# Kernel optimization log

Measured on AMD Instinct MI355X. Metric: run time of the kernel, lower is better.

Reference implementation:

```python
import jax, jax.numpy as jnp
import numpy as np

HEAD_SIZE = 1024
NUM_HEADS = 8
D_K = HEAD_SIZE // NUM_HEADS  # only used as the softmax scale; no head split in this module
B, S = 8, 2048


def setup_inputs() -> dict:
    key = jax.random.key(0)
    ks = jax.random.split(key, 11)
    d = HEAD_SIZE
    scale = 1.0 / np.sqrt(d)
    inp = {
        'query': jax.random.normal(ks[0], (B, S, d), dtype=jnp.float32),
        'key': jax.random.normal(ks[1], (B, S, d), dtype=jnp.float32),
        'value': jax.random.normal(ks[2], (B, S, d), dtype=jnp.float32),
        'Wq': jax.random.normal(ks[3], (d, d), dtype=jnp.float32) * scale,
        'bq': jnp.zeros((d,), dtype=jnp.float32),
        'Wk': jax.random.normal(ks[4], (d, d), dtype=jnp.float32) * scale,
        'bk': jnp.zeros((d,), dtype=jnp.float32),
        'Wv': jax.random.normal(ks[5], (d, d), dtype=jnp.float32) * scale,
        'bv': jnp.zeros((d,), dtype=jnp.float32),
        'Wo': jax.random.normal(ks[6], (d, d), dtype=jnp.float32) * scale,
        'bo': jnp.zeros((d,), dtype=jnp.float32),
    }
    return inp


def reference(query, key, value, Wq, bq, Wk, bk, Wv, bv, Wo, bo):
    # per-input linear projections (torch Linear: x @ W.T + b)
    q = jnp.einsum('bsd,ed->bse', query, Wq) + bq
    k = jnp.einsum('bsd,ed->bse', key, Wk) + bk
    v = jnp.einsum('bsd,ed->bse', value, Wv) + bv
    # NOTE: no head split in the original module; scale uses d_k = head_size/num_heads
    scores = jnp.einsum('bqd,bkd->bqk', q, k) / jnp.sqrt(jnp.float32(D_K))
    p_attn = jax.nn.softmax(scores, axis=-1)  # [B, S, S]
    x = jnp.einsum('bqk,bkd->bqd', p_attn, v)
    out = jnp.einsum('bsd,ed->bse', x, Wo) + bo
    return out
```

## Files before the change

### kernel.cpp

```cpp
#include <hip/hip_runtime.h>
#include <hip/hip_bf16.h>
#include <math.h>

typedef __bf16 bf16_t;
typedef _Float16 f16_t;
typedef bf16_t bf16x8 __attribute__((ext_vector_type(8)));
typedef bf16_t bf16x4 __attribute__((ext_vector_type(4)));
typedef f16_t  f16x8  __attribute__((ext_vector_type(8)));
typedef f16_t  f16x4  __attribute__((ext_vector_type(4)));
typedef float  f32x4  __attribute__((ext_vector_type(4)));

__global__ __launch_bounds__(256) void cvt_f32_bf16(
    const float* __restrict__ in, bf16_t* __restrict__ out, int n4) {
  int i = blockIdx.x * 256 + threadIdx.x;
  if (i >= n4) return;
  float4 v = ((const float4*)in)[i];
  bf16x4 o;
  o[0] = (bf16_t)v.x; o[1] = (bf16_t)v.y; o[2] = (bf16_t)v.z; o[3] = (bf16_t)v.w;
  ((bf16x4*)out)[i] = o;
}

__global__ __launch_bounds__(256) void transpose_bf16(
    const bf16_t* __restrict__ in, bf16_t* __restrict__ out, int R, int C) {
  __shared__ bf16_t t[64][65];
  size_t boff = (size_t)blockIdx.z * R * C;
  in += boff; out += boff;
  int r0 = blockIdx.y * 64, c0 = blockIdx.x * 64;
  int x = threadIdx.x & 63, y4 = threadIdx.x >> 6;
  #pragma unroll
  for (int yy = y4; yy < 64; yy += 4)
    t[yy][x] = in[(size_t)(r0 + yy) * C + c0 + x];
  __syncthreads();
  #pragma unroll
  for (int yy = y4; yy < 64; yy += 4)
    out[(size_t)(c0 + yy) * R + r0 + x] = t[x][yy];
}

__global__ __launch_bounds__(256) void softmax_rows_f16(f16_t* __restrict__ sc) {
  f16_t* rp = sc + (size_t)blockIdx.x * 2048;
  int tid = threadIdx.x;
  f16x8 v = ((const f16x8*)rp)[tid];
  float f[8];
  #pragma unroll
  for (int t = 0; t < 8; t++) f[t] = (float)v[t];

  float m = f[0];
  #pragma unroll
  for (int t = 1; t < 8; t++) m = fmaxf(m, f[t]);
  #pragma unroll
  for (int o = 32; o; o >>= 1) m = fmaxf(m, __shfl_xor(m, o));
  __shared__ float redm[4];
  if ((tid & 63) == 0) redm[tid >> 6] = m;
  __syncthreads();
  m = fmaxf(fmaxf(redm[0], redm[1]), fmaxf(redm[2], redm[3]));

  float s = 0.f;
  #pragma unroll
  for (int t = 0; t < 8; t++) { f[t] = __expf(f[t] - m); s += f[t]; }
  #pragma unroll
  for (int o = 32; o; o >>= 1) s += __shfl_xor(s, o);
  __shared__ float reds[4];
  if ((tid & 63) == 0) reds[tid >> 6] = s;
  __syncthreads();
  s = reds[0] + reds[1] + reds[2] + reds[3];
  float inv = 1.0f / s;

  bf16x8 o8;
  #pragma unroll
  for (int t = 0; t < 8; t++) o8[t] = (bf16_t)(f[t] * inv);
  ((bf16x8*)rp)[tid] = o8;
}

__device__ __forceinline__ void store4(float* p, float4 v) { *(float4*)p = v; }
__device__ __forceinline__ void store4(bf16_t* p, float4 v) {
  bf16x4 o; o[0] = (bf16_t)v.x; o[1] = (bf16_t)v.y;
  o[2] = (bf16_t)v.z; o[3] = (bf16_t)v.w; *(bf16x4*)p = o;
}
__device__ __forceinline__ void store4(f16_t* p, float4 v) {
  f16x4 o; o[0] = (f16_t)v.x; o[1] = (f16_t)v.y;
  o[2] = (f16_t)v.z; o[3] = (f16_t)v.w; *(f16x4*)p = o;
}

#define TM 128
#define TN 128
#define TK 64

__device__ __forceinline__ void load16_lds(const bf16_t* g, bf16_t* l) {
  __builtin_amdgcn_global_load_lds(
      (__attribute__((address_space(1))) void*)const_cast<bf16_t*>(g),
      (__attribute__((address_space(3))) void*)l, 16, 0, 0);
}

template <typename CT>
__global__ __launch_bounds__(256, 2) void gemm_bt(
    const bf16_t* __restrict__ A, int lda, size_t strA,
    const bf16_t* __restrict__ B, int ldb, size_t strB,
    CT* __restrict__ C, int ldc, size_t strC,
    const float* __restrict__ bias, float scale,
    int M, int N, int K) {
  __shared__ __align__(16) char smem[2][(TM * TK + TN * TK) * 2];

  A += (size_t)blockIdx.z * strA;
  B += (size_t)blockIdx.z * strB;
  C += (size_t)blockIdx.z * strC;
  int m0 = blockIdx.x * TM;
  int n0 = blockIdx.y * TN;
  int tid  = threadIdx.x;
  int lane = tid & 63;
  int wv   = tid >> 6;
  int wrow = wv >> 1;
  int wcol = wv & 1;

  f32x4 acc[4][4];
  #pragma unroll
  for (int i = 0; i < 4; i++)
    #pragma unroll
    for (int j = 0; j < 4; j++) acc[i][j] = (f32x4)0.f;

  int lrow = lane & 15;
  int lk   = (lane >> 4) * 8;

  auto stage = [&](int k0, int buf) {
    bf16_t* As = (bf16_t*)smem[buf];
    bf16_t* Bs = As + TM * TK;
    #pragma unroll
    for (int i = 0; i < 4; i++) {
      int chunk  = i * 4096 + wv * 1024;
      int lchunk = chunk + lane * 16;
      int row = lchunk >> 7;
      int kb  = (lchunk & 127) >> 1;
      load16_lds(A + (size_t)(m0 + row) * lda + k0 + kb, As + (chunk >> 1));
      load16_lds(B + (size_t)(n0 + row) * ldb + k0 + kb, Bs + (chunk >> 1));
    }
  };

  int nk = K / TK;
  stage(0, 0);
  __syncthreads();

  for (int kk = 0; kk < nk; kk++) {
    if (kk + 1 < nk) stage((kk + 1) * TK, (kk + 1) & 1);

    const bf16_t* As = (const bf16_t*)smem[kk & 1];
    const bf16_t* Bs = As + TM * TK;
    #pragma unroll
    for (int ks = 0; ks < TK; ks += 32) {
      bf16x8 af[4], bfr[4];
      #pragma unroll
      for (int i = 0; i < 4; i++)
        af[i] = *(const bf16x8*)&As[(wrow * 64 + i * 16 + lrow) * TK + ks + lk];
      #pragma unroll
      for (int j = 0; j < 4; j++)
        bfr[j] = *(const bf16x8*)&Bs[(wcol * 64 + j * 16 + lrow) * TK + ks + lk];
      #pragma unroll
      for (int i = 0; i < 4; i++)
        #pragma unroll
        for (int j = 0; j < 4; j++)
          acc[i][j] = __builtin_amdgcn_mfma_f32_16x16x32_bf16(af[i], bfr[j],
                                                              acc[i][j], 0, 0, 0);
    }
    __syncthreads();
  }

  float* Cs = (float*)smem[0];
  #pragma unroll
  for (int h = 0; h < 2; h++) {
    __syncthreads();
    if (wrow == h) {
      #pragma unroll
      for (int i = 0; i < 4; i++) {
        int lr = i * 16 + (lane >> 4) * 4;
        #pragma unroll
        for (int j = 0; j < 4; j++) {
          int lc = wcol * 64 + j * 16 + (lane & 15);
          #pragma unroll
          for (int r = 0; r < 4; r++)
            Cs[(lr + r) * 128 + lc] = acc[i][j][r];
        }
      }
    }
    __syncthreads();
    #pragma unroll
    for (int io = 0; io < 8; io++) {
      int idx = io * 256 + tid;
      int r   = idx >> 5;
      int c4  = (idx & 31) * 4;
      float4 v = *(const float4*)&Cs[r * 128 + c4];
      int grow = m0 + h * 64 + r;
      int gcol = n0 + c4;
      float4 bv = bias ? *(const float4*)&bias[gcol] : make_float4(0, 0, 0, 0);
      v.x = v.x * scale + bv.x; v.y = v.y * scale + bv.y;
      v.z = v.z * scale + bv.z; v.w = v.w * scale + bv.w;
      store4(C + (size_t)grow * ldc + gcol, v);
    }
  }
}

extern "C" void kernel_launch(void* const* d_in, const int* in_sizes, int n_in,
                              void* d_out, int out_size, void* d_ws, size_t ws_size,
                              hipStream_t stream) {
  const float* query = (const float*)d_in[0];
  const float* key_  = (const float*)d_in[1];
  const float* value = (const float*)d_in[2];
  const float* Wq = (const float*)d_in[3];
  const float* bq = (const float*)d_in[4];
  const float* Wk = (const float*)d_in[5];
  const float* bk = (const float*)d_in[6];
  const float* Wv = (const float*)d_in[7];
  const float* bv = (const float*)d_in[8];
  const float* Wo = (const float*)d_in[9];
  const float* bo = (const float*)d_in[10];
  float* out = (float*)d_out;

  const int Bb = 8, S = 2048, D = 1024;
  const int MS = Bb * S;
  const size_t ND = (size_t)MS * D;
  const size_t WD = (size_t)D * D;

  char* ws = (char*)d_ws;
  bf16_t* Wqb = (bf16_t*)ws;
  bf16_t* Wkb = Wqb + WD;
  bf16_t* Wvb = Wkb + WD;
  bf16_t* Wob = Wvb + WD;
  f16_t*  SC  = (f16_t*)(Wob + WD);
  bf16_t* IN  = (bf16_t*)SC;
  bf16_t* Qb  = (bf16_t*)((char*)SC + (size_t)Bb * S * S * 2);
  bf16_t* Kb  = Qb + ND;
  bf16_t* VT  = Kb;
  bf16_t* Xb  = Kb + ND;

  const int n4i = (int)(ND / 4), n4w = (int)(WD / 4);

  cvt_f32_bf16<<<dim3(n4w / 256), 256, 0, stream>>>(Wq, Wqb, n4w);
  cvt_f32_bf16<<<dim3(n4w / 256), 256, 0, stream>>>(Wk, Wkb, n4w);
  cvt_f32_bf16<<<dim3(n4w / 256), 256, 0, stream>>>(Wv, Wvb, n4w);
  cvt_f32_bf16<<<dim3(n4w / 256), 256, 0, stream>>>(Wo, Wob, n4w);

  dim3 pgrid(MS / TM, D / TN, 1);
  cvt_f32_bf16<<<dim3(n4i / 256), 256, 0, stream>>>(query, IN, n4i);
  gemm_bt<bf16_t><<<pgrid, 256, 0, stream>>>(
      IN, D, 0, Wqb, D, 0, Qb, D, 0, bq, 1.f, MS, D, D);
  cvt_f32_bf16<<<dim3(n4i / 256), 256, 0, stream>>>(key_, IN, n4i);
  gemm_bt<bf16_t><<<pgrid, 256, 0, stream>>>(
      IN, D, 0, Wkb, D, 0, Kb, D, 0, bk, 1.f, MS, D, D);
  cvt_f32_bf16<<<dim3(n4i / 256), 256, 0, stream>>>(value, IN, n4i);
  gemm_bt<bf16_t><<<pgrid, 256, 0, stream>>>(
      IN, D, 0, Wvb, D, 0, Xb, D, 0, bv, 1.f, MS, D, D);

  gemm_bt<f16_t><<<dim3(S / TM, S / TN, Bb), 256, 0, stream>>>(
      Qb, D, (size_t)S * D, Kb, D, (size_t)S * D, SC, S, (size_t)S * S,
      nullptr, 0.08838834764831845f, S, S, D);

  transpose_bf16<<<dim3(D / 64, S / 64, Bb), 256, 0, stream>>>(Xb, VT, S, D);

  softmax_rows_f16<<<dim3(Bb * S), 256, 0, stream>>>(SC);

  gemm_bt<bf16_t><<<dim3(S / TM, D / TN, Bb), 256, 0, stream>>>(
      (const bf16_t*)SC, S, (size_t)S * S, VT, S, (size_t)D * S,
      Xb, D, (size_t)S * D, nullptr, 1.f, S, D, S);

  gemm_bt<float><<<pgrid, 256, 0, stream>>>(
      Xb, D, 0, Wob, D, 0, out, D, 0, bo, 1.f, MS, D, D);
}
```

Before: 674.4 us.

## Replace 128x128 GEMM with 256x256 tile 8-wave kernel with swizzled LDS pipeline

Replaces the 128x128x64 GEMM with a 256x256x64 tile kernel using 512 threads (8 waves). It also adds an XOR-swizzled LDS layout, staging split into quarter-tile halves interleaved with MFMA phases under s_setprio, and manual waitcnt/barrier scheduling. Batched GEMMs put the batch index on blockIdx.x for better L2 locality. The aim is higher arithmetic intensity and overlap of global loads with MFMA. The cost is 128KB of LDS per block and higher register pressure, which may limit occupancy.

```diff
diff --git a/kernel.cpp b/kernel.cpp
--- a/kernel.cpp
+++ b/kernel.cpp
@@ -81,9 +81,9 @@
   o[2] = (f16_t)v.z; o[3] = (f16_t)v.w; *(f16x4*)p = o;
 }
 
-#define TM 128
-#define TN 128
-#define TK 64
+#define BM 256
+#define BN 256
+#define BK 64
 
 __device__ __forceinline__ void load16_lds(const bf16_t* g, bf16_t* l) {
   __builtin_amdgcn_global_load_lds(
@@ -92,101 +92,183 @@
 }
 
 template <typename CT>
-__global__ __launch_bounds__(256, 2) void gemm_bt(
+__global__ __launch_bounds__(512, 2) void gemm256(
     const bf16_t* __restrict__ A, int lda, size_t strA,
     const bf16_t* __restrict__ B, int ldb, size_t strB,
     CT* __restrict__ C, int ldc, size_t strC,
     const float* __restrict__ bias, float scale,
-    int M, int N, int K) {
-  __shared__ __align__(16) char smem[2][(TM * TK + TN * TK) * 2];
-
-  A += (size_t)blockIdx.z * strA;
-  B += (size_t)blockIdx.z * strB;
-  C += (size_t)blockIdx.z * strC;
-  int m0 = blockIdx.x * TM;
-  int n0 = blockIdx.y * TN;
+    int K, int batch_on_x) {
+  __shared__ __align__(16) char smem[2][65536];
+
+  int bz, mt, nt;
+  if (batch_on_x) { bz = blockIdx.x; nt = blockIdx.y; mt = blockIdx.z; }
+  else            { mt = blockIdx.x; nt = blockIdx.y; bz = blockIdx.z; }
+  A += (size_t)bz * strA;
+  B += (size_t)bz * strB;
+  C += (size_t)bz * strC;
+  int m0 = mt * BM, n0 = nt * BN;
   int tid  = threadIdx.x;
-  int lane = tid & 63;
-  int wv   = tid >> 6;
-  int wrow = wv >> 1;
-  int wcol = wv & 1;
-
-  f32x4 acc[4][4];
-  #pragma unroll
-  for (int i = 0; i < 4; i++)
+  int lane = tid & 63, wv = tid >> 6;
+  int wrow = wv >> 2;
+  int wcol = wv & 3;
+
+  f32x4 acc[8][4];
+  #pragma unroll
+  for (int i = 0; i < 8; i++)
     #pragma unroll
     for (int j = 0; j < 4; j++) acc[i][j] = (f32x4)0.f;
 
   int lrow = lane & 15;
-  int lk   = (lane >> 4) * 8;
-
-  auto stage = [&](int k0, int buf) {
-    bf16_t* As = (bf16_t*)smem[buf];
-    bf16_t* Bs = As + TM * TK;
-    #pragma unroll
-    for (int i = 0; i < 4; i++) {
-      int chunk  = i * 4096 + wv * 1024;
-      int lchunk = chunk + lane * 16;
-      int row = lchunk >> 7;
-      int kb  = (lchunk & 127) >> 1;
-      load16_lds(A + (size_t)(m0 + row) * lda + k0 + kb, As + (chunk >> 1));
-      load16_lds(B + (size_t)(n0 + row) * ldb + k0 + kb, Bs + (chunk >> 1));
+  int lk8  = (lane >> 4) * 8;
+  int xm   = (lrow & 8) << 2;
+
+  auto rd = [&](const char* base, int blk16, int kcol) -> bf16x8 {
+    int byte = (((blk16 << 1) + (kcol >> 5)) << 10)
+             + (lrow << 6) + (((kcol & 31) << 1) ^ xm);
+    return *(const bf16x8*)(base + byte);
+  };
+
+  auto stage_half = [&](int h) {
+    int th = h >> 2, hf = h & 3;
+    char* dstb = smem[th & 1] + hf * 16384;
+    const bf16_t* g; int rb, ld;
+    if (hf < 2) { g = A; rb = m0 + hf * 128;       ld = lda; }
+    else        { g = B; rb = n0 + (hf - 2) * 128; ld = ldb; }
+    int k0 = th * BK;
+    #pragma unroll
+    for (int q = 0; q < 2; q++) {
+      int l = q * 8192 + wv * 1024 + lane * 16;
+      int inner = l & 1023, s = l >> 10;
+      int rl   = ((s >> 1) << 4) | (inner >> 6);
+      int colb = (inner & 63) ^ (((inner >> 9) & 1) << 5);
+      int col  = ((s & 1) << 5) | (colb >> 1);
+      load16_lds(g + (size_t)(rb + rl) * ld + k0 + col,
+                 (bf16_t*)(dstb + q * 8192 + wv * 1024));
     }
   };
 
-  int nk = K / TK;
-  stage(0, 0);
-  __syncthreads();
-
-  for (int kk = 0; kk < nk; kk++) {
-    if (kk + 1 < nk) stage((kk + 1) * TK, (kk + 1) & 1);
-
-    const bf16_t* As = (const bf16_t*)smem[kk & 1];
-    const bf16_t* Bs = As + TM * TK;
-    #pragma unroll
-    for (int ks = 0; ks < TK; ks += 32) {
-      bf16x8 af[4], bfr[4];
-      #pragma unroll
-      for (int i = 0; i < 4; i++)
-        af[i] = *(const bf16x8*)&As[(wrow * 64 + i * 16 + lrow) * TK + ks + lk];
-      #pragma unroll
-      for (int j = 0; j < 4; j++)
-        bfr[j] = *(const bf16x8*)&Bs[(wcol * 64 + j * 16 + lrow) * TK + ks + lk];
-      #pragma unroll
-      for (int i = 0; i < 4; i++)
-        #pragma unroll
-        for (int j = 0; j < 4; j++)
-          acc[i][j] = __builtin_amdgcn_mfma_f32_16x16x32_bf16(af[i], bfr[j],
-                                                              acc[i][j], 0, 0, 0);
-    }
+  int nk = K / BK;
+
+  #pragma unroll
+  for (int h = 0; h < 6; ++h)
+    if (h < 4 * nk) stage_half(h);
+  asm volatile("s_waitcnt vmcnt(4)" ::: "memory");
+  asm volatile("s_barrier" ::: "memory");
+
+  bf16x8 a0[4][2], a1[4][2], bb[2][2];
+
+  for (int t = 0; t < nk; ++t) {
+    const char* Ab = smem[t & 1];
+    const char* Bb = smem[t & 1] + 32768;
+    int hb = 4 * t + 6;
+
+    #pragma unroll
+    for (int i = 0; i < 4; ++i)
+      #pragma unroll
+      for (int s = 0; s < 2; ++s)
+        a0[i][s] = rd(Ab, wrow * 8 + i, s * 32 + lk8);
+    #pragma unroll
+    for (int j = 0; j < 2; ++j)
+      #pragma unroll
+      for (int s = 0; s < 2; ++s)
+        bb[j][s] = rd(Bb, wcol * 4 + j, s * 32 + lk8);
+    if (hb + 0 < 4 * nk) stage_half(hb + 0);
+    asm volatile("s_barrier" ::: "memory");
+    asm volatile("s_waitcnt lgkmcnt(0)");
+    __builtin_amdgcn_s_setprio(1);
+    #pragma unroll
+    for (int i = 0; i < 4; ++i)
+      #pragma unroll
+      for (int j = 0; j < 2; ++j)
+        #pragma unroll
+        for (int s = 0; s < 2; ++s)
+          acc[i][j] = __builtin_amdgcn_mfma_f32_16x16x32_bf16(
+              a0[i][s], bb[j][s], acc[i][j], 0, 0, 0);
+    __builtin_amdgcn_s_setprio(0);
+    asm volatile("s_barrier" ::: "memory");
+
+    #pragma unroll
+    for (int i = 0; i < 4; ++i)
+      #pragma unroll
+      for (int s = 0; s < 2; ++s)
+        a1[i][s] = rd(Ab, wrow * 8 + 4 + i, s * 32 + lk8);
+    if (hb + 1 < 4 * nk) stage_half(hb + 1);
+    asm volatile("s_barrier" ::: "memory");
+    asm volatile("s_waitcnt lgkmcnt(0)");
+    __builtin_amdgcn_s_setprio(1);
+    #pragma unroll
+    for (int i = 0; i < 4; ++i)
+      #pragma unroll
+      for (int j = 0; j < 2; ++j)
+        #pragma unroll
+        for (int s = 0; s < 2; ++s)
+          acc[4 + i][j] = __builtin_amdgcn_mfma_f32_16x16x32_bf16(
+              a1[i][s], bb[j][s], acc[4 + i][j], 0, 0, 0);
+    __builtin_amdgcn_s_setprio(0);
+    asm volatile("s_barrier" ::: "memory");
+
+    #pragma unroll
+    for (int j = 0; j < 2; ++j)
+      #pragma unroll
+      for (int s = 0; s < 2; ++s)
+        bb[j][s] = rd(Bb, wcol * 4 + 2 + j, s * 32 + lk8);
+    if (hb + 2 < 4 * nk) stage_half(hb + 2);
+    asm volatile("s_barrier" ::: "memory");
+    asm volatile("s_waitcnt lgkmcnt(0)");
+    __builtin_amdgcn_s_setprio(1);
+    #pragma unroll
+    for (int i = 0; i < 4; ++i)
+      #pragma unroll
+      for (int j = 0; j < 2; ++j)
+        #pragma unroll
+        for (int s = 0; s < 2; ++s)
+          acc[4 + i][2 + j] = __builtin_amdgcn_mfma_f32_16x16x32_bf16(
+              a1[i][s], bb[j][s], acc[4 + i][2 + j], 0, 0, 0);
+    __builtin_amdgcn_s_setprio(0);
+    asm volatile("s_barrier" ::: "memory");
+
+    if (hb + 3 < 4 * nk) stage_half(hb + 3);
+    asm volatile("s_barrier" ::: "memory");
+    __builtin_amdgcn_s_setprio(1);
+    #pragma unroll
+    for (int i = 0; i < 4; ++i)
+      #pragma unroll
+      for (int j = 0; j < 2; ++j)
+        #pragma unroll
+        for (int s = 0; s < 2; ++s)
+          acc[i][2 + j] = __builtin_amdgcn_mfma_f32_16x16x32_bf16(
+              a0[i][s], bb[j][s], acc[i][2 + j], 0, 0, 0);
+    __builtin_amdgcn_s_setprio(0);
+    if (t < nk - 2) asm volatile("s_waitcnt vmcnt(4)" ::: "memory");
+    else            asm volatile("s_waitcnt vmcnt(0)" ::: "memory");
+    asm volatile("s_barrier" ::: "memory");
+  }
+
+  float* Cs = (float*)smem[0];
+  #pragma unroll
+  for (int q = 0; q < 4; ++q) {
     __syncthreads();
-  }
-
-  float* Cs = (float*)smem[0];
-  #pragma unroll
-  for (int h = 0; h < 2; h++) {
-    __syncthreads();
-    if (wrow == h) {
-      #pragma unroll
-      for (int i = 0; i < 4; i++) {
-        int lr = i * 16 + (lane >> 4) * 4;
-        #pragma unroll
-        for (int j = 0; j < 4; j++) {
+    if (wrow == (q >> 1)) {
+      #pragma unroll
+      for (int ii = 0; ii < 4; ++ii) {
+        int i = (q & 1) * 4 + ii;
+        int lr = ii * 16 + (lane >> 4) * 4;
+        #pragma unroll
+        for (int j = 0; j < 4; ++j) {
           int lc = wcol * 64 + j * 16 + (lane & 15);
           #pragma unroll
-          for (int r = 0; r < 4; r++)
-            Cs[(lr + r) * 128 + lc] = acc[i][j][r];
+          for (int r = 0; r < 4; ++r)
+            Cs[(lr + r) * 260 + lc] = acc[i][j][r];
         }
       }
     }
     __syncthreads();
     #pragma unroll
-    for (int io = 0; io < 8; io++) {
-      int idx = io * 256 + tid;
-      int r   = idx >> 5;
-      int c4  = (idx & 31) * 4;
-      float4 v = *(const float4*)&Cs[r * 128 + c4];
-      int grow = m0 + h * 64 + r;
+    for (int io = 0; io < 8; ++io) {
+      int idx = io * 512 + tid;
+      int r = idx >> 6, c4 = (idx & 63) * 4;
+      float4 v = *(const float4*)&Cs[r * 260 + c4];
+      int grow = m0 + q * 64 + r;
       int gcol = n0 + c4;
       float4 bv = bias ? *(const float4*)&bias[gcol] : make_float4(0, 0, 0, 0);
       v.x = v.x * scale + bv.x; v.y = v.y * scale + bv.y;
@@ -230,35 +312,36 @@
   bf16_t* Xb  = Kb + ND;
 
   const int n4i = (int)(ND / 4), n4w = (int)(WD / 4);
+  dim3 blk(512);
 
   cvt_f32_bf16<<<dim3(n4w / 256), 256, 0, stream>>>(Wq, Wqb, n4w);
   cvt_f32_bf16<<<dim3(n4w / 256), 256, 0, stream>>>(Wk, Wkb, n4w);
   cvt_f32_bf16<<<dim3(n4w / 256), 256, 0, stream>>>(Wv, Wvb, n4w);
   cvt_f32_bf16<<<dim3(n4w / 256), 256, 0, stream>>>(Wo, Wob, n4w);
 
-  dim3 pgrid(MS / TM, D / TN, 1);
+  dim3 pgrid(MS / BM, D / BN, 1);
   cvt_f32_bf16<<<dim3(n4i / 256), 256, 0, stream>>>(query, IN, n4i);
-  gemm_bt<bf16_t><<<pgrid, 256, 0, stream>>>(
-      IN, D, 0, Wqb, D, 0, Qb, D, 0, bq, 1.f, MS, D, D);
+  gemm256<bf16_t><<<pgrid, blk, 0, stream>>>(
+      IN, D, 0, Wqb, D, 0, Qb, D, 0, bq, 1.f, D, 0);
   cvt_f32_bf16<<<dim3(n4i / 256), 256, 0, stream>>>(key_, IN, n4i);
-  gemm_bt<bf16_t><<<pgrid, 256, 0, stream>>>(
-      IN, D, 0, Wkb, D, 0, Kb, D, 0, bk, 1.f, MS, D, D);
+  gemm256<bf16_t><<<pgrid, blk, 0, stream>>>(
+      IN, D, 0, Wkb, D, 0, Kb, D, 0, bk, 1.f, D, 0);
   cvt_f32_bf16<<<dim3(n4i / 256), 256, 0, stream>>>(value, IN, n4i);
-  gemm_bt<bf16_t><<<pgrid, 256, 0, stream>>>(
-      IN, D, 0, Wvb, D, 0, Xb, D, 0, bv, 1.f, MS, D, D);
-
-  gemm_bt<f16_t><<<dim3(S / TM, S / TN, Bb), 256, 0, stream>>>(
+  gemm256<bf16_t><<<pgrid, blk, 0, stream>>>(
+      IN, D, 0, Wvb, D, 0, Xb, D, 0, bv, 1.f, D, 0);
+
+  gemm256<f16_t><<<dim3(Bb, S / BN, S / BM), blk, 0, stream>>>(
       Qb, D, (size_t)S * D, Kb, D, (size_t)S * D, SC, S, (size_t)S * S,
-      nullptr, 0.08838834764831845f, S, S, D);
+      nullptr, 0.08838834764831845f, D, 1);
 
   transpose_bf16<<<dim3(D / 64, S / 64, Bb), 256, 0, stream>>>(Xb, VT, S, D);
 
   softmax_rows_f16<<<dim3(Bb * S), 256, 0, stream>>>(SC);
 
-  gemm_bt<bf16_t><<<dim3(S / TM, D / TN, Bb), 256, 0, stream>>>(
+  gemm256<bf16_t><<<dim3(Bb, D / BN, S / BM), blk, 0, stream>>>(
       (const bf16_t*)SC, S, (size_t)S * S, VT, S, (size_t)D * S,
-      Xb, D, (size_t)S * D, nullptr, 1.f, S, D, S);
-
-  gemm_bt<float><<<pgrid, 256, 0, stream>>>(
-      Xb, D, 0, Wob, D, 0, out, D, 0, bo, 1.f, MS, D, D);
-}
+      Xb, D, (size_t)S * D, nullptr, 1.f, S, 1);
+
+  gemm256<float><<<pgrid, blk, 0, stream>>>(
+      Xb, D, 0, Wob, D, 0, out, D, 0, bo, 1.f, D, 0);
+}
```

Measured after the change: 574.3 us. 1.17x faster.
